# Kernel tuning notes

Measured on AMD Instinct MI355X. Metric: run time of the kernel, lower is better.

Reference implementation:

```python
import jax, jax.numpy as jnp
import numpy as np

B, T, D, H = 8, 1024, 1024, 16
HD = D // H  # per-head dim = 64


def setup_inputs() -> dict:
    key = jax.random.key(0)
    ks = jax.random.split(key, 9)
    s = 1.0 / np.sqrt(D)
    return {
        "x": jax.random.normal(ks[0], (B, T, D), dtype=jnp.float32),
        "y": jax.random.normal(ks[1], (B, T, D), dtype=jnp.float32),
        "Wq": jax.random.normal(ks[2], (D, D), dtype=jnp.float32) * s,
        "Wk": jax.random.normal(ks[3], (D, D), dtype=jnp.float32) * s,
        "Wv": jax.random.normal(ks[4], (D, D), dtype=jnp.float32) * s,
        "Wox": jax.random.normal(ks[5], (D, D), dtype=jnp.float32) * s,
        "box": jnp.zeros((D,), dtype=jnp.float32),
        "Woy": jax.random.normal(ks[6], (D, D), dtype=jnp.float32) * s,
        "boy": jnp.zeros((D,), dtype=jnp.float32),
    }


def _split_heads(t):
    # (B, T, D) -> (B, H, T, HD)
    return t.reshape(B, T, H, HD).transpose(0, 2, 1, 3)


def _merge_heads(t):
    # (B, H, T, HD) -> (B, T, D)
    return t.transpose(0, 2, 1, 3).reshape(B, T, D)


def reference(x, y, Wq, Wk, Wv, Wox, box, Woy, boy):
    # Shared Q/K/V projections applied cross-wise (torch Linear: t @ W.T)
    q_sx = _split_heads(y @ Wq.T)  # queries from y attend over x
    k_sx = _split_heads(x @ Wk.T)
    v_sx = _split_heads(x @ Wv.T)
    q_sy = _split_heads(x @ Wq.T)  # queries from x attend over y
    k_sy = _split_heads(y @ Wk.T)
    v_sy = _split_heads(y @ Wv.T)

    scale = jnp.sqrt(jnp.asarray(HD, dtype=x.dtype))
    scores_x = jnp.einsum('bhqd,bhkd->bhqk', q_sx, k_sx)
    scores_y = jnp.einsum('bhqd,bhkd->bhqk', q_sy, k_sy)
    # cat on head dim + reshape(B,2,H,T,T) + mean over dim 1 == per-head average
    attn = jax.nn.softmax((scores_x + scores_y) * (0.5 / scale), axis=-1)

    out1 = _merge_heads(jnp.einsum('bhqk,bhkd->bhqd', attn, v_sx))
    out2 = _merge_heads(jnp.einsum('bhqk,bhkd->bhqd', attn, v_sy))
    out1 = out1 @ Wox.T + box
    out2 = out2 @ Woy.T + boy
    return (out1, out2)
```

## Files before the change

kernel.cpp:

```cpp
#include <hip/hip_runtime.h>
#include <stdint.h>

#define DEV __device__ __forceinline__

typedef __bf16 bf16x8 __attribute__((ext_vector_type(8)));
typedef __bf16 bf16x4 __attribute__((ext_vector_type(4)));
typedef short s16x4 __attribute__((ext_vector_type(4)));
typedef float f32x4 __attribute__((ext_vector_type(4)));
typedef unsigned short u16;
typedef u16 u16x4v __attribute__((ext_vector_type(4)));
typedef u16 u16x8 __attribute__((ext_vector_type(8)));
typedef uint32_t u32;

static constexpr int Bb = 8, Tt = 1024, Dd = 1024, Hh = 16;
static constexpr int BT = Bb * Tt;

DEV u16 f2bf(float f) {
  u32 u = __float_as_uint(f);
  u32 r = (u + 0x7FFFu + ((u >> 16) & 1u)) >> 16;
  return (u16)r;
}
DEV u32 cvtpk(float lo, float hi) {
  u32 r;
  asm("v_cvt_pk_bf16_f32 %0, %1, %2" : "=v"(r) : "v"(lo), "v"(hi));
  return r;
}
DEV void gload_lds16(const void* g, void* lds) {
  __builtin_amdgcn_global_load_lds(
      (const __attribute__((address_space(1))) void*)g,
      (__attribute__((address_space(3))) void*)lds,
      16, 0, 0);
}
DEV f32x4 MFMA16(bf16x4 a, bf16x4 b, f32x4 c) {
#if __has_builtin(__builtin_amdgcn_mfma_f32_16x16x16_bf16)
  return __builtin_amdgcn_mfma_f32_16x16x16_bf16(a, b, c, 0, 0, 0);
#elif __has_builtin(__builtin_amdgcn_mfma_f32_16x16x16bf16_1k)
  union { bf16x4 b; s16x4 s; } ua, ub;
  ua.b = a; ub.b = b;
  return __builtin_amdgcn_mfma_f32_16x16x16bf16_1k(ua.s, ub.s, c, 0, 0, 0);
#else
  asm("v_mfma_f32_16x16x16_bf16 %0, %1, %2, %0" : "+v"(c) : "v"(a), "v"(b));
  return c;
#endif
}

__global__ __launch_bounds__(256) void k_cvt(const float* __restrict__ x,
                                             const float* __restrict__ y,
                                             const float* __restrict__ Wq,
                                             const float* __restrict__ Wk,
                                             const float* __restrict__ Wv,
                                             const float* __restrict__ Wox,
                                             const float* __restrict__ Woy,
                                             u16* __restrict__ xb,
                                             u16* __restrict__ yb,
                                             u16* __restrict__ Wb) {
  const int z = blockIdx.z;
  const float* src;
  u16* dst;
  int n8;
  if (z == 0)      { src = x; dst = xb; n8 = BT * Dd / 8; }
  else if (z == 1) { src = y; dst = yb; n8 = BT * Dd / 8; }
  else {
    src = (z == 2) ? Wq : (z == 3) ? Wk : (z == 4) ? Wv : (z == 5) ? Wox : Woy;
    dst = Wb + (size_t)(z - 2) * (Dd * Dd);
    n8 = Dd * Dd / 8;
  }
  int i = blockIdx.x * blockDim.x + threadIdx.x;
  int stride = gridDim.x * blockDim.x;
  for (; i < n8; i += stride) {
    const float4* p = reinterpret_cast<const float4*>(src) + (size_t)i * 2;
    float4 a = p[0], b = p[1];
    u16x8 o;
    o[0] = f2bf(a.x); o[1] = f2bf(a.y); o[2] = f2bf(a.z); o[3] = f2bf(a.w);
    o[4] = f2bf(b.x); o[5] = f2bf(b.y); o[6] = f2bf(b.z); o[7] = f2bf(b.w);
    reinterpret_cast<u16x8*>(dst)[i] = o;
  }
}

template <int MODE, int GX, int GY>
__global__ __launch_bounds__(512, 2) void k_gemm256(
    const u16* __restrict__ xb, const u16* __restrict__ yb,
    const u16* __restrict__ W0,
    u16* __restrict__ Qb, u16* __restrict__ Kb, u16* __restrict__ Vtg,
    const float* __restrict__ bx, const float* __restrict__ by,
    float* __restrict__ out) {
  __shared__ alignas(16) u16 As[2][256 * 64];
  __shared__ alignas(16) u16 Bs[2][256 * 64];
  const int tid = threadIdx.x;
  const int l = tid & 63, wid = tid >> 6;
  const int wr = wid >> 2, wc = wid & 3;

  constexpr int NWG = GX * GY * 2;
  const int d0b = blockIdx.x;
  const int wk = (d0b & 7) * (NWG / 8) + (d0b >> 3);
  const int tz = wk / (GX * GY);
  const int rr = wk % (GX * GY);
  const int ty = rr / GX, tx = rr % GX;
  const int m0 = ty * 256, n0 = tx * 256;

  const u16* Ag;
  const u16* Wg;
  if constexpr (MODE == 0) {
    Ag = tz ? yb : xb;
    Wg = W0;
  } else {
    Ag = xb + tz * 64;
    Wg = W0 + (size_t)tz * (Dd * Dd);
  }

  auto stageA = [&](int buf, int kt, int half) {
#pragma unroll
    for (int i = 0; i < 2; ++i) {
      int idx = i * 512 + tid;
      int row = idx >> 3, P = idx & 7, G = P ^ (row & 7);
      const u16* src;
      if constexpr (MODE == 0) {
        src = Ag + (size_t)(m0 + half * 128 + row) * 1024 + kt * 64 + G * 8;
      } else {
        int m = m0 + half * 128 + row;
        src = Ag + ((size_t)((m >> 10) * 16 + kt) * 1024 + (m & 1023)) * 128 + G * 8;
      }
      gload_lds16(src, &As[buf][half * 8192 + idx * 8]);
    }
  };
  auto stageB = [&](int buf, int kt, int half) {
#pragma unroll
    for (int i = 0; i < 2; ++i) {
      int idx = i * 512 + tid;
      int row = idx >> 3, P = idx & 7, G = P ^ (row & 7);
      gload_lds16(Wg + (size_t)(n0 + half * 128 + row) * 1024 + kt * 64 + G * 8,
                  &Bs[buf][half * 8192 + idx * 8]);
    }
  };
  auto ldA = [&](int b, int m, int kk) -> bf16x8 {
    int row = wr * 128 + m * 16 + (l & 15);
    int P = (kk * 4 + (l >> 4)) ^ (row & 7);
    return *reinterpret_cast<const bf16x8*>(&As[b][row * 64 + P * 8]);
  };
  auto ldB = [&](int b, int n, int kk) -> bf16x8 {
    int row = wc * 64 + n * 16 + (l & 15);
    int P = (kk * 4 + (l >> 4)) ^ (row & 7);
    return *reinterpret_cast<const bf16x8*>(&Bs[b][row * 64 + P * 8]);
  };

  f32x4 acc[8][4] = {};

  stageA(0, 0, 0); stageB(0, 0, 0); stageA(0, 0, 1); stageB(0, 0, 1);
  asm volatile("s_waitcnt vmcnt(0)" ::: "memory");
  __builtin_amdgcn_s_barrier();

  for (int kt = 0; kt < 16; ++kt) {
    const int b = kt & 1, nb = b ^ 1;
    const bool pf = kt < 15;
    bf16x8 bfr[4][2], afr[4][2];

#pragma unroll
    for (int n = 0; n < 4; ++n) { bfr[n][0] = ldB(b, n, 0); bfr[n][1] = ldB(b, n, 1); }
#pragma unroll
    for (int m = 0; m < 4; ++m) { afr[m][0] = ldA(b, m, 0); afr[m][1] = ldA(b, m, 1); }
    if (pf) { stageA(nb, kt + 1, 0); stageB(nb, kt + 1, 0); }
    __builtin_amdgcn_s_barrier();
    asm volatile("s_waitcnt lgkmcnt(0)" ::: "memory");
    __builtin_amdgcn_sched_barrier(0);
    __builtin_amdgcn_s_setprio(1);
#pragma unroll
    for (int m = 0; m < 4; ++m)
#pragma unroll
      for (int n = 0; n < 4; ++n)
#pragma unroll
        for (int kk = 0; kk < 2; ++kk)
          acc[m][n] = __builtin_amdgcn_mfma_f32_16x16x32_bf16(
              afr[m][kk], bfr[n][kk], acc[m][n], 0, 0, 0);
    __builtin_amdgcn_s_setprio(0);
    __builtin_amdgcn_s_barrier();

#pragma unroll
    for (int m = 0; m < 4; ++m) { afr[m][0] = ldA(b, 4 + m, 0); afr[m][1] = ldA(b, 4 + m, 1); }
    if (pf) { stageA(nb, kt + 1, 1); stageB(nb, kt + 1, 1); }
    __builtin_amdgcn_s_barrier();
    asm volatile("s_waitcnt lgkmcnt(0)" ::: "memory");
    __builtin_amdgcn_sched_barrier(0);
    __builtin_amdgcn_s_setprio(1);
#pragma unroll
    for (int m = 0; m < 4; ++m)
#pragma unroll
      for (int n = 0; n < 4; ++n)
#pragma unroll
        for (int kk = 0; kk < 2; ++kk)
          acc[4 + m][n] = __builtin_amdgcn_mfma_f32_16x16x32_bf16(
              afr[m][kk], bfr[n][kk], acc[4 + m][n], 0, 0, 0);
    __builtin_amdgcn_s_setprio(0);
    asm volatile("s_waitcnt vmcnt(0)" ::: "memory");
    __builtin_amdgcn_s_barrier();
  }

#pragma unroll
  for (int m = 0; m < 8; ++m)
#pragma unroll
    for (int n = 0; n < 4; ++n) {
      int rb = m0 + wr * 128 + m * 16 + (l >> 4) * 4;
      int col = n0 + wc * 64 + n * 16 + (l & 15);
      if constexpr (MODE == 0) {
        int proj = col >> 10;
        int slot = ((proj == 0) ? 1 : 0) ^ tz;
        int bh = ((rb >> 10) << 4) + ((col >> 6) & 15);
        int t0 = rb & 1023;
        int dc = col & 63;
        if (proj == 2) {
          int newoff = (t0 >> 5) * 32 + ((t0 >> 2) & 3) * 8 + ((t0 >> 4) & 1) * 4;
          u16x4v pk;
#pragma unroll
          for (int j = 0; j < 4; ++j) pk[j] = f2bf(acc[m][n][j]);
          *reinterpret_cast<u16x4v*>(Vtg + (size_t)bh * 131072 +
                                     (size_t)(slot * 64 + dc) * 1024 + newoff) = pk;
        } else {
          float sc = (proj == 0) ? 0.09016994f : 1.0f;
          u16* dstp = (proj ? Kb : Qb) + (size_t)bh * 131072 + (size_t)t0 * 128 + slot * 64 + dc;
#pragma unroll
          for (int j = 0; j < 4; ++j) dstp[(size_t)j * 128] = f2bf(acc[m][n][j] * sc);
        }
      } else {
        const float* bias = tz ? by : bx;
        float* dstp = out + (size_t)tz * BT * Dd;
        float bv = bias[col];
#pragma unroll
        for (int j = 0; j < 4; ++j)
          dstp[(size_t)(rb + j) * 1024 + col] = acc[m][n][j] + bv;
      }
    }
}

__global__ __launch_bounds__(512, 4) void k_attn(const u16* __restrict__ Q,
                                                 const u16* __restrict__ K,
                                                 const u16* __restrict__ Vt,
                                                 u16* __restrict__ O) {
  __shared__ alignas(16) u16 Ks[2][8192];
  __shared__ alignas(16) u16 Vs[2][8192];
  const int tid = threadIdx.x;
  const int l = tid & 63, w = tid >> 6;
  const int bid = blockIdx.x;
  const int xcd = bid & 7, li = bid >> 3;
  const int bh = xcd + 8 * (li >> 3);
  const int qblk = li & 7;
  const int q0 = qblk * 128 + w * 16;
  const size_t base = (size_t)bh * 131072;

  bf16x8 qf[4];
#pragma unroll
  for (int dc = 0; dc < 4; ++dc)
    qf[dc] = *reinterpret_cast<const bf16x8*>(
        Q + base + (size_t)(q0 + (l & 15)) * 128 + dc * 32 + (l >> 4) * 8);

  const u16* kp[2];
  const u16* vp[2];
#pragma unroll
  for (int i = 0; i < 2; ++i) {
    int idx = i * 512 + tid;
    {
      int dc = idx >> 8, kv = (idx >> 2) & 63, pp = idx & 3, g = pp ^ ((kv >> 1) & 3);
      kp[i] = K + base + (size_t)kv * 128 + dc * 32 + g * 8;
    }
    {
      int c = idx >> 9, d = (idx >> 2) & 127, pp = idx & 3, g = pp ^ ((d >> 1) & 3);
      vp[i] = Vt + base + (size_t)d * 1024 + c * 32 + g * 8;
    }
  }
  const int i0 = tid * 8, i1 = (512 + tid) * 8;

  const int koff = (l & 15) * 32 + (((l >> 4) ^ (((l & 15) >> 1) & 3))) * 8;

  auto stage = [&](int buf, int kv0) {
    gload_lds16(kp[0] + (size_t)kv0 * 128, &Ks[buf][i0]);
    gload_lds16(kp[1] + (size_t)kv0 * 128, &Ks[buf][i1]);
    gload_lds16(vp[0] + kv0, &Vs[buf][i0]);
    gload_lds16(vp[1] + kv0, &Vs[buf][i1]);
  };

  union { u16x4v u; bf16x4 v; } onesu;
#pragma unroll
  for (int j = 0; j < 4; ++j) onesu.u[j] = 0x3F80;
  const bf16x4 ones = onesu.v;

  float m_run = -3e38f;
  f32x4 Oa[8] = {};
  f32x4 Ol = {};

  stage(0, 0);
  __syncthreads();

  for (int t16 = 0; t16 < 16; ++t16) {
    const int cur = t16 & 1;
    if (t16 < 15) stage(cur ^ 1, (t16 + 1) * 64);

    f32x4 S[4];
    __builtin_amdgcn_s_setprio(1);
#pragma unroll
    for (int t = 0; t < 4; ++t) {
      f32x4 s = {};
#pragma unroll
      for (int dc = 0; dc < 4; ++dc) {
        bf16x8 kb = *reinterpret_cast<const bf16x8*>(&Ks[cur][dc * 2048 + t * 512 + koff]);
        s = __builtin_amdgcn_mfma_f32_16x16x32_bf16(kb, qf[dc], s, 0, 0, 0);
      }
      S[t] = s;
    }
    __builtin_amdgcn_s_setprio(0);

    float mxl = fmaxf(fmaxf(fmaxf(S[0][0], S[0][1]), fmaxf(S[0][2], S[0][3])),
                      fmaxf(fmaxf(S[1][0], S[1][1]), fmaxf(S[1][2], S[1][3])));
    float mx2 = fmaxf(fmaxf(fmaxf(S[2][0], S[2][1]), fmaxf(S[2][2], S[2][3])),
                      fmaxf(fmaxf(S[3][0], S[3][1]), fmaxf(S[3][2], S[3][3])));
    mxl = fmaxf(mxl, mx2);

    const int grow = __any(mxl > m_run + 11.0f);
    float mn = m_run;
    if (grow) {
      float mx = fmaxf(mxl, __shfl_xor(mxl, 16));
      mx = fmaxf(mx, __shfl_xor(mx, 32));
      mn = fmaxf(m_run, mx);
      float alpha = __builtin_exp2f(m_run - mn);
      m_run = mn;
      Ol *= alpha;
#pragma unroll
      for (int n = 0; n < 8; ++n) Oa[n] *= alpha;
    }
#pragma unroll
    for (int t = 0; t < 4; ++t)
#pragma unroll
      for (int j = 0; j < 4; ++j)
        S[t][j] = __builtin_exp2f(S[t][j] - mn);

    union { u32 w2[2]; bf16x4 v; } pb[4];
#pragma unroll
    for (int t = 0; t < 4; ++t) {
      pb[t].w2[0] = cvtpk(S[t][0], S[t][1]);
      pb[t].w2[1] = cvtpk(S[t][2], S[t][3]);
    }

    asm volatile("s_nop 1");
    __builtin_amdgcn_s_setprio(1);
#pragma unroll
    for (int t = 0; t < 4; ++t) Ol = MFMA16(ones, pb[t].v, Ol);
#pragma unroll
    for (int c = 0; c < 2; ++c)
#pragma unroll
      for (int n = 0; n < 8; ++n) {
        bf16x8 av = *reinterpret_cast<const bf16x8*>(&Vs[cur][c * 4096 + n * 512 + koff]);
        bf16x4 a0 = __builtin_shufflevector(av, av, 0, 1, 2, 3);
        bf16x4 a1 = __builtin_shufflevector(av, av, 4, 5, 6, 7);
        Oa[n] = MFMA16(a0, pb[2 * c].v, Oa[n]);
        Oa[n] = MFMA16(a1, pb[2 * c + 1].v, Oa[n]);
      }
    __builtin_amdgcn_s_setprio(0);

    __syncthreads();
  }
  asm volatile("s_nop 7");

  float inv = 1.0f / Ol[0];
#pragma unroll
  for (int n = 0; n < 8; ++n) {
    u16x4v pk;
#pragma unroll
    for (int j = 0; j < 4; ++j) pk[j] = f2bf(Oa[n][j] * inv);
    *reinterpret_cast<u16x4v*>(
        O + base + (size_t)(q0 + (l & 15)) * 128 + n * 16 + (l >> 4) * 4) = pk;
  }
}

extern "C" void kernel_launch(void* const* d_in, const int* in_sizes, int n_in,
                              void* d_out, int out_size, void* d_ws, size_t ws_size,
                              hipStream_t stream) {
  const float* x   = (const float*)d_in[0];
  const float* y   = (const float*)d_in[1];
  const float* Wq  = (const float*)d_in[2];
  const float* Wk  = (const float*)d_in[3];
  const float* Wv  = (const float*)d_in[4];
  const float* Wox = (const float*)d_in[5];
  const float* box = (const float*)d_in[6];
  const float* Woy = (const float*)d_in[7];
  const float* boy = (const float*)d_in[8];

  u16* ws = (u16*)d_ws;
  size_t off = 0;
  u16* xb  = ws + off; off += (size_t)BT * Dd;
  u16* yb  = ws + off; off += (size_t)BT * Dd;
  u16* Wqb = ws + off; off += (size_t)Dd * Dd;
  u16* Wkb = ws + off; off += (size_t)Dd * Dd;
  u16* Wvb = ws + off; off += (size_t)Dd * Dd;
  u16* Woxb = ws + off; off += (size_t)Dd * Dd;
  u16* Woyb = ws + off; off += (size_t)Dd * Dd;
  (void)Wkb; (void)Wvb; (void)Woyb;
  const size_t attn_elems = (size_t)Bb * Hh * Tt * 128;
  u16* Qb = ws + off; off += attn_elems;
  u16* Kb = ws + off; off += attn_elems;
  u16* Vb = ws + off; off += attn_elems;
  u16* Ob = ws + off; off += attn_elems;

  k_cvt<<<dim3(512, 1, 7), dim3(256), 0, stream>>>(x, y, Wq, Wk, Wv, Wox, Woy, xb, yb, Wqb);

  k_gemm256<0, 12, 32><<<dim3(768), dim3(512), 0, stream>>>(
      xb, yb, Wqb, Qb, Kb, Vb, nullptr, nullptr, nullptr);

  k_attn<<<dim3(1024), dim3(512), 0, stream>>>(Qb, Kb, Vb, Ob);

  k_gemm256<1, 4, 32><<<dim3(256), dim3(512), 0, stream>>>(
      Ob, nullptr, Woxb, nullptr, nullptr, nullptr, box, boy, (float*)d_out);
}
```

Measured before the change: 263.5 us.

## Process two query tiles per wave in attention to reuse K/V LDS loads

```diff
diff --git a/kernel.cpp b/kernel.cpp
--- a/kernel.cpp
+++ b/kernel.cpp
@@ -230,7 +230,7 @@
     }
 }
 
-__global__ __launch_bounds__(512, 4) void k_attn(const u16* __restrict__ Q,
+__global__ __launch_bounds__(512, 2) void k_attn(const u16* __restrict__ Q,
                                                  const u16* __restrict__ K,
                                                  const u16* __restrict__ Vt,
                                                  u16* __restrict__ O) {
@@ -240,16 +240,19 @@
   const int l = tid & 63, w = tid >> 6;
   const int bid = blockIdx.x;
   const int xcd = bid & 7, li = bid >> 3;
-  const int bh = xcd + 8 * (li >> 3);
-  const int qblk = li & 7;
-  const int q0 = qblk * 128 + w * 16;
+  const int bh = xcd + 8 * (li >> 2);
+  const int qblk = li & 3;
+  const int q0w = qblk * 256 + w * 32;
   const size_t base = (size_t)bh * 131072;
 
-  bf16x8 qf[4];
-#pragma unroll
-  for (int dc = 0; dc < 4; ++dc)
-    qf[dc] = *reinterpret_cast<const bf16x8*>(
-        Q + base + (size_t)(q0 + (l & 15)) * 128 + dc * 32 + (l >> 4) * 8);
+  bf16x8 qf0[4], qf1[4];
+#pragma unroll
+  for (int dc = 0; dc < 4; ++dc) {
+    qf0[dc] = *reinterpret_cast<const bf16x8*>(
+        Q + base + (size_t)(q0w + (l & 15)) * 128 + dc * 32 + (l >> 4) * 8);
+    qf1[dc] = *reinterpret_cast<const bf16x8*>(
+        Q + base + (size_t)(q0w + 16 + (l & 15)) * 128 + dc * 32 + (l >> 4) * 8);
+  }
 
   const u16* kp[2];
   const u16* vp[2];
@@ -282,8 +285,8 @@
   const bf16x4 ones = onesu.v;
 
   float m_run = -3e38f;
-  f32x4 Oa[8] = {};
-  f32x4 Ol = {};
+  f32x4 Oa0[8] = {}, Oa1[8] = {};
+  f32x4 Ol0 = {}, Ol1 = {};
 
   stage(0, 0);
   __syncthreads();
@@ -292,25 +295,30 @@
     const int cur = t16 & 1;
     if (t16 < 15) stage(cur ^ 1, (t16 + 1) * 64);
 
-    f32x4 S[4];
+    f32x4 S0[4], S1[4];
     __builtin_amdgcn_s_setprio(1);
 #pragma unroll
     for (int t = 0; t < 4; ++t) {
-      f32x4 s = {};
+      f32x4 s0 = {}, s1 = {};
 #pragma unroll
       for (int dc = 0; dc < 4; ++dc) {
         bf16x8 kb = *reinterpret_cast<const bf16x8*>(&Ks[cur][dc * 2048 + t * 512 + koff]);
-        s = __builtin_amdgcn_mfma_f32_16x16x32_bf16(kb, qf[dc], s, 0, 0, 0);
+        s0 = __builtin_amdgcn_mfma_f32_16x16x32_bf16(kb, qf0[dc], s0, 0, 0, 0);
+        s1 = __builtin_amdgcn_mfma_f32_16x16x32_bf16(kb, qf1[dc], s1, 0, 0, 0);
       }
-      S[t] = s;
+      S0[t] = s0; S1[t] = s1;
     }
     __builtin_amdgcn_s_setprio(0);
 
-    float mxl = fmaxf(fmaxf(fmaxf(S[0][0], S[0][1]), fmaxf(S[0][2], S[0][3])),
-                      fmaxf(fmaxf(S[1][0], S[1][1]), fmaxf(S[1][2], S[1][3])));
-    float mx2 = fmaxf(fmaxf(fmaxf(S[2][0], S[2][1]), fmaxf(S[2][2], S[2][3])),
-                      fmaxf(fmaxf(S[3][0], S[3][1]), fmaxf(S[3][2], S[3][3])));
-    mxl = fmaxf(mxl, mx2);
+    float mxa = fmaxf(fmaxf(fmaxf(S0[0][0], S0[0][1]), fmaxf(S0[0][2], S0[0][3])),
+                      fmaxf(fmaxf(S0[1][0], S0[1][1]), fmaxf(S0[1][2], S0[1][3])));
+    float mxb = fmaxf(fmaxf(fmaxf(S0[2][0], S0[2][1]), fmaxf(S0[2][2], S0[2][3])),
+                      fmaxf(fmaxf(S0[3][0], S0[3][1]), fmaxf(S0[3][2], S0[3][3])));
+    float mxc = fmaxf(fmaxf(fmaxf(S1[0][0], S1[0][1]), fmaxf(S1[0][2], S1[0][3])),
+                      fmaxf(fmaxf(S1[1][0], S1[1][1]), fmaxf(S1[1][2], S1[1][3])));
+    float mxd = fmaxf(fmaxf(fmaxf(S1[2][0], S1[2][1]), fmaxf(S1[2][2], S1[2][3])),
+                      fmaxf(fmaxf(S1[3][0], S1[3][1]), fmaxf(S1[3][2], S1[3][3])));
+    float mxl = fmaxf(fmaxf(mxa, mxb), fmaxf(mxc, mxd));
 
     const int grow = __any(mxl > m_run + 11.0f);
     float mn = m_run;
@@ -320,27 +328,34 @@
       mn = fmaxf(m_run, mx);
       float alpha = __builtin_exp2f(m_run - mn);
       m_run = mn;
-      Ol *= alpha;
-#pragma unroll
-      for (int n = 0; n < 8; ++n) Oa[n] *= alpha;
+      Ol0 *= alpha; Ol1 *= alpha;
+#pragma unroll
+      for (int n = 0; n < 8; ++n) { Oa0[n] *= alpha; Oa1[n] *= alpha; }
     }
 #pragma unroll
     for (int t = 0; t < 4; ++t)
 #pragma unroll
-      for (int j = 0; j < 4; ++j)
-        S[t][j] = __builtin_exp2f(S[t][j] - mn);
-
-    union { u32 w2[2]; bf16x4 v; } pb[4];
+      for (int j = 0; j < 4; ++j) {
+        S0[t][j] = __builtin_exp2f(S0[t][j] - mn);
+        S1[t][j] = __builtin_exp2f(S1[t][j] - mn);
+      }
+
+    union { u32 w2[2]; bf16x4 v; } pb0[4], pb1[4];
 #pragma unroll
     for (int t = 0; t < 4; ++t) {
-      pb[t].w2[0] = cvtpk(S[t][0], S[t][1]);
-      pb[t].w2[1] = cvtpk(S[t][2], S[t][3]);
+      pb0[t].w2[0] = cvtpk(S0[t][0], S0[t][1]);
+      pb0[t].w2[1] = cvtpk(S0[t][2], S0[t][3]);
+      pb1[t].w2[0] = cvtpk(S1[t][0], S1[t][1]);
+      pb1[t].w2[1] = cvtpk(S1[t][2], S1[t][3]);
     }
 
     asm volatile("s_nop 1");
     __builtin_amdgcn_s_setprio(1);
 #pragma unroll
-    for (int t = 0; t < 4; ++t) Ol = MFMA16(ones, pb[t].v, Ol);
+    for (int t = 0; t < 4; ++t) {
+      Ol0 = MFMA16(ones, pb0[t].v, Ol0);
+      Ol1 = MFMA16(ones, pb1[t].v, Ol1);
+    }
 #pragma unroll
     for (int c = 0; c < 2; ++c)
 #pragma unroll
@@ -348,8 +363,10 @@
         bf16x8 av = *reinterpret_cast<const bf16x8*>(&Vs[cur][c * 4096 + n * 512 + koff]);
         bf16x4 a0 = __builtin_shufflevector(av, av, 0, 1, 2, 3);
         bf16x4 a1 = __builtin_shufflevector(av, av, 4, 5, 6, 7);
-        Oa[n] = MFMA16(a0, pb[2 * c].v, Oa[n]);
-        Oa[n] = MFMA16(a1, pb[2 * c + 1].v, Oa[n]);
+        Oa0[n] = MFMA16(a0, pb0[2 * c].v, Oa0[n]);
+        Oa0[n] = MFMA16(a1, pb0[2 * c + 1].v, Oa0[n]);
+        Oa1[n] = MFMA16(a0, pb1[2 * c].v, Oa1[n]);
+        Oa1[n] = MFMA16(a1, pb1[2 * c + 1].v, Oa1[n]);
       }
     __builtin_amdgcn_s_setprio(0);
 
@@ -357,14 +374,20 @@
   }
   asm volatile("s_nop 7");
 
-  float inv = 1.0f / Ol[0];
+  float inv0 = 1.0f / Ol0[0];
+  float inv1 = 1.0f / Ol1[0];
 #pragma unroll
   for (int n = 0; n < 8; ++n) {
-    u16x4v pk;
-#pragma unroll
-    for (int j = 0; j < 4; ++j) pk[j] = f2bf(Oa[n][j] * inv);
+    u16x4v pk0, pk1;
+#pragma unroll
+    for (int j = 0; j < 4; ++j) {
+      pk0[j] = f2bf(Oa0[n][j] * inv0);
+      pk1[j] = f2bf(Oa1[n][j] * inv1);
+    }
     *reinterpret_cast<u16x4v*>(
-        O + base + (size_t)(q0 + (l & 15)) * 128 + n * 16 + (l >> 4) * 4) = pk;
+        O + base + (size_t)(q0w + (l & 15)) * 128 + n * 16 + (l >> 4) * 4) = pk0;
+    *reinterpret_cast<u16x4v*>(
+        O + base + (size_t)(q0w + 16 + (l & 15)) * 128 + n * 16 + (l >> 4) * 4) = pk1;
   }
 }
 
@@ -402,7 +425,7 @@
   k_gemm256<0, 12, 32><<<dim3(768), dim3(512), 0, stream>>>(
       xb, yb, Wqb, Qb, Kb, Vb, nullptr, nullptr, nullptr);
 
-  k_attn<<<dim3(1024), dim3(512), 0, stream>>>(Qb, Kb, Vb, Ob);
+  k_attn<<<dim3(512), dim3(512), 0, stream>>>(Qb, Kb, Vb, Ob);
 
   k_gemm256<1, 4, 32><<<dim3(256), dim3(512), 0, stream>>>(
       Ob, nullptr, Woxb, nullptr, nullptr, nullptr, box, boy, (float*)d_out);
```

Result: slower. 289.0 us (+9.7%).

## Restructure GEMM main loop into 8-phase quadrant schedule with half-tile prefetch

Applied to the files above, without the earlier changes.

```diff
diff --git a/kernel.cpp b/kernel.cpp
--- a/kernel.cpp
+++ b/kernel.cpp
@@ -88,7 +88,8 @@
   __shared__ alignas(16) u16 Bs[2][256 * 64];
   const int tid = threadIdx.x;
   const int l = tid & 63, wid = tid >> 6;
-  const int wr = wid >> 2, wc = wid & 3;
+  const int wm = wid >> 2;
+  const int wn = wid & 3;
 
   constexpr int NWG = GX * GY * 2;
   const int d0b = blockIdx.x;
@@ -132,102 +133,137 @@
                   &Bs[buf][half * 8192 + idx * 8]);
     }
   };
-  auto ldA = [&](int b, int m, int kk) -> bf16x8 {
-    int row = wr * 128 + m * 16 + (l & 15);
+  auto ldAq = [&](int bb, int MH, int m2, int kk) -> bf16x8 {
+    int row = MH * 128 + wm * 64 + m2 * 16 + (l & 15);
     int P = (kk * 4 + (l >> 4)) ^ (row & 7);
-    return *reinterpret_cast<const bf16x8*>(&As[b][row * 64 + P * 8]);
+    return *reinterpret_cast<const bf16x8*>(&As[bb][row * 64 + P * 8]);
   };
-  auto ldB = [&](int b, int n, int kk) -> bf16x8 {
-    int row = wc * 64 + n * 16 + (l & 15);
+  auto ldBq = [&](int bb, int NH, int n2, int kk) -> bf16x8 {
+    int row = NH * 128 + wn * 32 + n2 * 16 + (l & 15);
     int P = (kk * 4 + (l >> 4)) ^ (row & 7);
-    return *reinterpret_cast<const bf16x8*>(&Bs[b][row * 64 + P * 8]);
+    return *reinterpret_cast<const bf16x8*>(&Bs[bb][row * 64 + P * 8]);
   };
 
-  f32x4 acc[8][4] = {};
+  f32x4 acc[2][2][4][2] = {};
 
   stageA(0, 0, 0); stageB(0, 0, 0); stageA(0, 0, 1); stageB(0, 0, 1);
+  stageA(1, 1, 0); stageB(1, 1, 0);
   asm volatile("s_waitcnt vmcnt(0)" ::: "memory");
   __builtin_amdgcn_s_barrier();
 
-  for (int kt = 0; kt < 16; ++kt) {
-    const int b = kt & 1, nb = b ^ 1;
-    const bool pf = kt < 15;
-    bf16x8 bfr[4][2], afr[4][2];
-
-#pragma unroll
-    for (int n = 0; n < 4; ++n) { bfr[n][0] = ldB(b, n, 0); bfr[n][1] = ldB(b, n, 1); }
-#pragma unroll
-    for (int m = 0; m < 4; ++m) { afr[m][0] = ldA(b, m, 0); afr[m][1] = ldA(b, m, 1); }
-    if (pf) { stageA(nb, kt + 1, 0); stageB(nb, kt + 1, 0); }
-    __builtin_amdgcn_s_barrier();
-    asm volatile("s_waitcnt lgkmcnt(0)" ::: "memory");
-    __builtin_amdgcn_sched_barrier(0);
-    __builtin_amdgcn_s_setprio(1);
-#pragma unroll
-    for (int m = 0; m < 4; ++m)
-#pragma unroll
-      for (int n = 0; n < 4; ++n)
-#pragma unroll
-        for (int kk = 0; kk < 2; ++kk)
-          acc[m][n] = __builtin_amdgcn_mfma_f32_16x16x32_bf16(
-              afr[m][kk], bfr[n][kk], acc[m][n], 0, 0, 0);
-    __builtin_amdgcn_s_setprio(0);
-    __builtin_amdgcn_s_barrier();
-
-#pragma unroll
-    for (int m = 0; m < 4; ++m) { afr[m][0] = ldA(b, 4 + m, 0); afr[m][1] = ldA(b, 4 + m, 1); }
-    if (pf) { stageA(nb, kt + 1, 1); stageB(nb, kt + 1, 1); }
-    __builtin_amdgcn_s_barrier();
-    asm volatile("s_waitcnt lgkmcnt(0)" ::: "memory");
-    __builtin_amdgcn_sched_barrier(0);
-    __builtin_amdgcn_s_setprio(1);
-#pragma unroll
-    for (int m = 0; m < 4; ++m)
-#pragma unroll
-      for (int n = 0; n < 4; ++n)
-#pragma unroll
-        for (int kk = 0; kk < 2; ++kk)
-          acc[4 + m][n] = __builtin_amdgcn_mfma_f32_16x16x32_bf16(
-              afr[m][kk], bfr[n][kk], acc[4 + m][n], 0, 0, 0);
-    __builtin_amdgcn_s_setprio(0);
-    asm volatile("s_waitcnt vmcnt(0)" ::: "memory");
-    __builtin_amdgcn_s_barrier();
-  }
-
-#pragma unroll
-  for (int m = 0; m < 8; ++m)
-#pragma unroll
-    for (int n = 0; n < 4; ++n) {
-      int rb = m0 + wr * 128 + m * 16 + (l >> 4) * 4;
-      int col = n0 + wc * 64 + n * 16 + (l & 15);
-      if constexpr (MODE == 0) {
-        int proj = col >> 10;
-        int slot = ((proj == 0) ? 1 : 0) ^ tz;
-        int bh = ((rb >> 10) << 4) + ((col >> 6) & 15);
-        int t0 = rb & 1023;
-        int dc = col & 63;
-        if (proj == 2) {
-          int newoff = (t0 >> 5) * 32 + ((t0 >> 2) & 3) * 8 + ((t0 >> 4) & 1) * 4;
-          u16x4v pk;
-#pragma unroll
-          for (int j = 0; j < 4; ++j) pk[j] = f2bf(acc[m][n][j]);
-          *reinterpret_cast<u16x4v*>(Vtg + (size_t)bh * 131072 +
-                                     (size_t)(slot * 64 + dc) * 1024 + newoff) = pk;
-        } else {
-          float sc = (proj == 0) ? 0.09016994f : 1.0f;
-          u16* dstp = (proj ? Kb : Qb) + (size_t)bh * 131072 + (size_t)t0 * 128 + slot * 64 + dc;
-#pragma unroll
-          for (int j = 0; j < 4; ++j) dstp[(size_t)j * 128] = f2bf(acc[m][n][j] * sc);
+#define RDA(bb, MH)                                                         \
+  _Pragma("unroll") for (int m2 = 0; m2 < 4; ++m2)                          \
+      _Pragma("unroll") for (int kk = 0; kk < 2; ++kk)                      \
+          afr[m2][kk] = ldAq(bb, MH, m2, kk)
+#define RDB(bb, NH)                                                         \
+  _Pragma("unroll") for (int n2 = 0; n2 < 2; ++n2)                          \
+      _Pragma("unroll") for (int kk = 0; kk < 2; ++kk)                      \
+          bfr[n2][kk] = ldBq(bb, NH, n2, kk)
+#define MM(MH, NH)                                                          \
+  __builtin_amdgcn_s_barrier();                                             \
+  asm volatile("s_waitcnt lgkmcnt(0)" ::: "memory");                        \
+  __builtin_amdgcn_sched_barrier(0);                                        \
+  __builtin_amdgcn_s_setprio(1);                                            \
+  _Pragma("unroll") for (int m2 = 0; m2 < 4; ++m2)                          \
+      _Pragma("unroll") for (int n2 = 0; n2 < 2; ++n2)                      \
+          _Pragma("unroll") for (int kk = 0; kk < 2; ++kk)                  \
+              acc[MH][NH][m2][n2] = __builtin_amdgcn_mfma_f32_16x16x32_bf16(\
+                  afr[m2][kk], bfr[n2][kk], acc[MH][NH][m2][n2], 0, 0, 0);  \
+  __builtin_amdgcn_s_setprio(0)
+#define WAIT6 do { if (tail) asm volatile("s_waitcnt vmcnt(0)" ::: "memory"); \
+                   else      asm volatile("s_waitcnt vmcnt(6)" ::: "memory"); } while (0)
+#define WAIT8 do { if (tail) asm volatile("s_waitcnt vmcnt(0)" ::: "memory"); \
+                   else      asm volatile("s_waitcnt vmcnt(8)" ::: "memory"); } while (0)
+#define BAR __builtin_amdgcn_s_barrier()
+
+  for (int it = 0; it < 8; ++it) {
+    const int t0 = 2 * it;
+    const bool tail = (it == 7);
+    bf16x8 bfr[2][2], afr[4][2];
+
+    RDB(0, 0); RDA(0, 0);
+    stageB(1, t0 + 1, 1);
+    MM(0, 0);
+    WAIT6;
+    BAR;
+    RDA(0, 1);
+    stageA(1, t0 + 1, 1);
+    MM(1, 0);
+    BAR;
+    RDB(0, 1); RDA(0, 0);
+    if (!tail) stageB(0, t0 + 2, 0);
+    MM(0, 1);
+    BAR;
+    RDA(0, 1);
+    if (!tail) stageA(0, t0 + 2, 0);
+    MM(1, 1);
+    WAIT8;
+    BAR;
+    RDB(1, 0); RDA(1, 0);
+    if (!tail) stageB(0, t0 + 2, 1);
+    MM(0, 0);
+    WAIT6;
+    BAR;
+    RDA(1, 1);
+    if (!tail) stageA(0, t0 + 2, 1);
+    MM(1, 0);
+    BAR;
+    RDB(1, 1); RDA(1, 0);
+    if (!tail) stageB(1, t0 + 3, 0);
+    MM(0, 1);
+    BAR;
+    RDA(1, 1);
+    if (!tail) stageA(1, t0 + 3, 0);
+    MM(1, 1);
+    if (!tail) asm volatile("s_waitcnt vmcnt(8)" ::: "memory");
+    BAR;
+  }
+#undef RDA
+#undef RDB
+#undef MM
+#undef WAIT6
+#undef WAIT8
+#undef BAR
+
+#pragma unroll
+  for (int mh = 0; mh < 2; ++mh)
+#pragma unroll
+    for (int nh = 0; nh < 2; ++nh)
+#pragma unroll
+      for (int m2 = 0; m2 < 4; ++m2)
+#pragma unroll
+        for (int n2 = 0; n2 < 2; ++n2) {
+          int rb = m0 + mh * 128 + wm * 64 + m2 * 16 + (l >> 4) * 4;
+          int col = n0 + nh * 128 + wn * 32 + n2 * 16 + (l & 15);
+          f32x4 av = acc[mh][nh][m2][n2];
+          if constexpr (MODE == 0) {
+            int proj = col >> 10;
+            int slot = ((proj == 0) ? 1 : 0) ^ tz;
+            int bh = ((rb >> 10) << 4) + ((col >> 6) & 15);
+            int t0q = rb & 1023;
+            int dc = col & 63;
+            if (proj == 2) {
+              int newoff = (t0q >> 5) * 32 + ((t0q >> 2) & 3) * 8 + ((t0q >> 4) & 1) * 4;
+              u16x4v pk;
+#pragma unroll
+              for (int j = 0; j < 4; ++j) pk[j] = f2bf(av[j]);
+              *reinterpret_cast<u16x4v*>(Vtg + (size_t)bh * 131072 +
+                                         (size_t)(slot * 64 + dc) * 1024 + newoff) = pk;
+            } else {
+              float sc = (proj == 0) ? 0.09016994f : 1.0f;
+              u16* dstp = (proj ? Kb : Qb) + (size_t)bh * 131072 + (size_t)t0q * 128 + slot * 64 + dc;
+#pragma unroll
+              for (int j = 0; j < 4; ++j) dstp[(size_t)j * 128] = f2bf(av[j] * sc);
+            }
+          } else {
+            const float* bias = tz ? by : bx;
+            float* dstp = out + (size_t)tz * BT * Dd;
+            float bv = bias[col];
+#pragma unroll
+            for (int j = 0; j < 4; ++j)
+              dstp[(size_t)(rb + j) * 1024 + col] = av[j] + bv;
+          }
         }
-      } else {
-        const float* bias = tz ? by : bx;
-        float* dstp = out + (size_t)tz * BT * Dd;
-        float bv = bias[col];
-#pragma unroll
-        for (int j = 0; j < 4; ++j)
-          dstp[(size_t)(rb + j) * 1024 + col] = acc[m][n][j] + bv;
-      }
-    }
 }
 
 __global__ __launch_bounds__(512, 4) void k_attn(const u16* __restrict__ Q,
```

Result: slower. 284.0 us (+7.8%).
